# Optimization experiments

Hardware: AMD Instinct MI355X
Metric: run time of the kernel (lower is better)

Reference implementation:

```python
import jax, jax.numpy as jnp
import numpy as np

B, T, H = 64, 320, 256
D = 2 * H  # input_size; cat([cw, cell]) has dim 2*D which must equal 4*H


def setup_inputs() -> dict:
    key = jax.random.key(0)
    ks = jax.random.split(key, 10)
    sD = 1.0 / np.sqrt(D)
    sG = 1.0 / np.sqrt(2 * D)
    sH = 1.0 / np.sqrt(H)
    f32 = jnp.float32
    n = lambda k, shape, s: jax.random.normal(k, shape, dtype=f32) * s
    return {
        "v": n(ks[0], (B, T, D), 1.0),
        "W1": n(ks[1], (D, D), sD), "b1": jnp.zeros((D,), f32),
        "W2": n(ks[2], (D, D), sD), "b2": jnp.zeros((D,), f32),
        "Wg": n(ks[3], (2 * D, 2 * D), sG), "bg": jnp.zeros((2 * D,), f32),
        "Wih_f": n(ks[4], (3 * H, 2 * D), sG), "Whh_f": n(ks[5], (3 * H, H), sH),
        "bih_f": jnp.zeros((3 * H,), f32), "bhh_f": jnp.zeros((3 * H,), f32),
        "Wih_b": n(ks[6], (3 * H, 2 * D), sG), "Whh_b": n(ks[7], (3 * H, H), sH),
        "bih_b": jnp.zeros((3 * H,), f32), "bhh_b": jnp.zeros((3 * H,), f32),
    }


def _gru_cell(x, h, Wih, Whh, bih, bhh):
    # torch GRUCell math: gates ordered (r, z, n)
    gi = x @ Wih.T + bih          # (B, 3H)
    gh = h @ Whh.T + bhh          # (B, 3H)
    i_r, i_z, i_n = jnp.split(gi, 3, axis=-1)
    h_r, h_z, h_n = jnp.split(gh, 3, axis=-1)
    r = jax.nn.sigmoid(i_r + h_r)
    z = jax.nn.sigmoid(i_z + h_z)
    n = jnp.tanh(i_n + r * h_n)
    return (1.0 - z) * n + z * h


def reference(v, W1, b1, W2, b2, Wg, bg,
              Wih_f, Whh_f, bih_f, bhh_f,
              Wih_b, Whh_b, bih_b, bhh_b):
    # context_mult = linear2(v) is identical every timestep -> hoist out of loop
    cm = jnp.einsum('btd,ed->bte', v, W2) + b2          # (B, T, D)

    def step(carry, cw):
        hf, hb = carry                                   # (B, H) each
        cwm = cw @ W1.T + b1                             # (B, D)
        f = jnp.tanh(cwm[:, None, :] + cm)               # (B, T, D)
        scores = jnp.einsum('bd,btd->bt', cw, f)         # (B, T)
        attn = jax.nn.softmax(scores, axis=-1)
        cell = jnp.einsum('bt,btd->bd', attn, v)         # (B, D)
        pg = jnp.concatenate([cw, cell], axis=-1)        # (B, 2D) == (B, 4H)
        gate = jax.nn.sigmoid(pg @ Wg.T + bg)
        gi = pg * gate
        # length-1 bidirectional GRU step: each direction sees the same input
        hf2 = _gru_cell(gi, hf, Wih_f, Whh_f, bih_f, bhh_f)
        hb2 = _gru_cell(gi, hb, Wih_b, Whh_b, bih_b, bhh_b)
        return (hf2, hb2), jnp.concatenate([hf2, hb2], axis=-1)

    h0 = jnp.zeros((v.shape[0], H), v.dtype)
    _, hs = jax.lax.scan(step, (h0, h0), jnp.swapaxes(v, 0, 1))
    return hs  # (T, B, 2H)
```

## Files before the change

kernel.cpp:

```cpp
#include <hip/hip_runtime.h>

typedef unsigned short u16;
typedef __fp16 h2 __attribute__((ext_vector_type(2)));
typedef __attribute__((ext_vector_type(8))) short bf16x8;
typedef __attribute__((ext_vector_type(4))) float f32x4;

__device__ __forceinline__ float fast_exp(float x) { return __expf(x); }
__device__ __forceinline__ float fast_rcp(float x) { return __builtin_amdgcn_rcpf(x); }
__device__ __forceinline__ float fast_tanh(float x) {
  float e = fast_exp(2.0f * x);
  return 1.0f - 2.0f * fast_rcp(e + 1.0f);
}
__device__ __forceinline__ float fast_sigmoid(float x) {
  return fast_rcp(1.0f + fast_exp(-x));
}
__device__ __forceinline__ u16 f2bf(float x) {
  unsigned u = __float_as_uint(x);
  return (u16)((u + 0x7fffu + ((u >> 16) & 1u)) >> 16);
}

__global__ __launch_bounds__(256)
void k_cvt(const float* __restrict__ src, u16* __restrict__ dst, int n4)
{
  int i = blockIdx.x * 256 + threadIdx.x;
  if (i < n4) {
    float4 x = ((const float4*)src)[i];
    ushort4 o;
    o.x = f2bf(x.x); o.y = f2bf(x.y); o.z = f2bf(x.z); o.w = f2bf(x.w);
    ((ushort4*)dst)[i] = o;
  }
}

template<int EXPOUT>
__global__ __launch_bounds__(256)
void k_gemm(const float* __restrict__ A1, int K1, int map1,
            const float* __restrict__ W,
            const float* __restrict__ bias,
            float* __restrict__ C, int N, int K, int Tc, int t0)
{
  __shared__ float As[16][128];
  __shared__ float Bs[16][128];
  const int tid = threadIdx.x;
  const int m0 = blockIdx.x * 128;
  const int n0 = blockIdx.y * 128;
  const int q = tid & 3;

  const float* pA1[2];
  const float* pW[2];
#pragma unroll
  for (int r = 0; r < 2; ++r) {
    int row = m0 + r * 64 + (tid >> 2);
    int ar1 = map1 ? ((row / Tc) * 320 + t0 + row % Tc) : row;
    pA1[r] = A1 + (size_t)ar1 * K1;
    pW[r] = W + (size_t)(n0 + r * 64 + (tid >> 2)) * K;
  }

  float acc[8][8];
#pragma unroll
  for (int i = 0; i < 8; ++i)
#pragma unroll
    for (int j = 0; j < 8; ++j) acc[i][j] = 0.f;
  const int tm = (tid & 15) * 8;
  const int tn = (tid >> 4) * 8;

  for (int k0 = 0; k0 < K; k0 += 16) {
#pragma unroll
    for (int r = 0; r < 2; ++r) {
      int row = r * 64 + (tid >> 2);
      int kk = k0 + q * 4;
      float4 x = *(const float4*)(pA1[r] + kk);
      As[q * 4 + 0][row] = x.x;
      As[q * 4 + 1][row] = x.y;
      As[q * 4 + 2][row] = x.z;
      As[q * 4 + 3][row] = x.w;
      float4 y = *(const float4*)(pW[r] + kk);
      Bs[q * 4 + 0][row] = y.x;
      Bs[q * 4 + 1][row] = y.y;
      Bs[q * 4 + 2][row] = y.z;
      Bs[q * 4 + 3][row] = y.w;
    }
    __syncthreads();
#pragma unroll
    for (int k = 0; k < 16; ++k) {
      float a[8], b[8];
      *(float4*)&a[0] = *(const float4*)&As[k][tm];
      *(float4*)&a[4] = *(const float4*)&As[k][tm + 4];
      *(float4*)&b[0] = *(const float4*)&Bs[k][tn];
      *(float4*)&b[4] = *(const float4*)&Bs[k][tn + 4];
#pragma unroll
      for (int i = 0; i < 8; ++i)
#pragma unroll
        for (int j = 0; j < 8; ++j) acc[i][j] += a[i] * b[j];
    }
    __syncthreads();
  }
#pragma unroll
  for (int i = 0; i < 8; ++i) {
    int m = m0 + tm + i;
    float* Crow = C + (size_t)m * N + n0 + tn;
#pragma unroll
    for (int j = 0; j < 8; ++j) {
      float x = acc[i][j] + bias[n0 + tn + j];
      Crow[j] = EXPOUT ? fast_exp(2.0f * x) : x;
    }
  }
}

template<int MODE>
__global__ __launch_bounds__(256)
void k_mgemm(const u16* __restrict__ A1, int K1, int map1,
             const u16* __restrict__ A2,
             const u16* __restrict__ W16, const float* __restrict__ bias,
             const float* __restrict__ E1, const float* __restrict__ E2,
             void* __restrict__ Cout, int N, int K, int Tc, int t0)
{
  __shared__ alignas(16) u16 As[128][40];
  __shared__ alignas(16) u16 Bs[128][40];
  const int tid = threadIdx.x;
  const int m0 = blockIdx.x * 128;
  const int n0 = blockIdx.y * 128;
  const int wave = tid >> 6, lane = tid & 63;
  const int wm = (wave & 1) * 64, wn = (wave >> 1) * 64;
  const int K2 = K - K1;

  const u16* pA1r[2];
  const u16* pA2r[2];
  const u16* pWr[2];
#pragma unroll
  for (int r = 0; r < 2; ++r) {
    int row = r * 64 + (tid >> 2);
    int gm = m0 + row;
    int ar1 = map1 ? ((gm / Tc) * 320 + t0 + gm % Tc) : gm;
    pA1r[r] = A1 + (size_t)ar1 * K1;
    pA2r[r] = A2 ? (A2 + (size_t)gm * K2) : pA1r[r];
    pWr[r] = W16 + (size_t)(n0 + row) * K;
  }

  f32x4 acc[4][4];
#pragma unroll
  for (int a = 0; a < 4; ++a)
#pragma unroll
    for (int b = 0; b < 4; ++b) acc[a][b] = (f32x4){0.f, 0.f, 0.f, 0.f};

  const int lrow = lane & 15, lq = lane >> 4;

  for (int k0 = 0; k0 < K; k0 += 32) {
#pragma unroll
    for (int r = 0; r < 2; ++r) {
      int row = r * 64 + (tid >> 2);
      int kk = k0 + (tid & 3) * 8;
      const u16* s = (kk < K1) ? (pA1r[r] + kk) : (pA2r[r] + (kk - K1));
      *(int4*)&As[row][(tid & 3) * 8] = *(const int4*)s;
      *(int4*)&Bs[row][(tid & 3) * 8] = *(const int4*)(pWr[r] + kk);
    }
    __syncthreads();
    bf16x8 av[4], bv[4];
#pragma unroll
    for (int f = 0; f < 4; ++f) {
      av[f] = *(const bf16x8*)&As[wm + f * 16 + lrow][lq * 8];
      bv[f] = *(const bf16x8*)&Bs[wn + f * 16 + lrow][lq * 8];
    }
#pragma unroll
    for (int mf = 0; mf < 4; ++mf)
#pragma unroll
      for (int nf = 0; nf < 4; ++nf)
        acc[mf][nf] = __builtin_amdgcn_mfma_f32_16x16x32_bf16(
            av[mf], bv[nf], acc[mf][nf], 0, 0, 0);
    __syncthreads();
  }

  const int c = lane & 15, rg = lane >> 4;
#pragma unroll
  for (int mf = 0; mf < 4; ++mf) {
#pragma unroll
    for (int r = 0; r < 4; ++r) {
      int m = m0 + wm + mf * 16 + rg * 4 + r;
      int vrow = map1 ? ((m / Tc) * 320 + t0 + m % Tc) : m;
#pragma unroll
      for (int nf = 0; nf < 4; ++nf) {
        int n = n0 + wn + nf * 16 + c;
        float x = acc[mf][nf][r] + bias[n];
        if (MODE == 1) {
          float pg = (n < 512) ? E1[(size_t)vrow * 512 + n]
                               : E2[(size_t)m * 512 + (n - 512)];
          ((u16*)Cout)[(size_t)m * N + n] = f2bf(pg * fast_sigmoid(x));
        } else {
          ((float*)Cout)[(size_t)m * N + n] = x;
        }
      }
    }
  }
}

__global__ __launch_bounds__(256)
void k_scores(const float* __restrict__ v, const float* __restrict__ Ecwm,
              const float* __restrict__ Fcm, float* __restrict__ sc,
              int Tc, int t0)
{
  __shared__ float vs[32][68], fs[32][68], cs[32][68];
  const int b = blockIdx.x;
  const int tl0 = blockIdx.y * 32;
  const int s0 = blockIdx.z * 32;
  const int tid = threadIdx.x;
  const int tx = tid & 15, ty = tid >> 4;
  const float* srcV = v    + ((size_t)b * 320 + t0 + tl0) * 512;
  const float* srcF = Ecwm + ((size_t)b * Tc + tl0) * 512;
  const float* srcC = Fcm  + ((size_t)b * 320 + s0) * 512;
  float a00 = 0, a01 = 0, a10 = 0, a11 = 0;
  float vs0 = 0, vs1 = 0;
  for (int d0 = 0; d0 < 512; d0 += 64) {
#pragma unroll
    for (int r = 0; r < 2; ++r) {
      int f = r * 256 + tid;
      int row = f >> 4, qq = f & 15;
      *(float4*)&vs[row][qq * 4] = *(const float4*)(srcV + (size_t)row * 512 + d0 + qq * 4);
      *(float4*)&fs[row][qq * 4] = *(const float4*)(srcF + (size_t)row * 512 + d0 + qq * 4);
      *(float4*)&cs[row][qq * 4] = *(const float4*)(srcC + (size_t)row * 512 + d0 + qq * 4);
    }
    __syncthreads();
#pragma unroll 4
    for (int d = 0; d < 64; ++d) {
      float c0 = cs[tx][d], c1 = cs[tx + 16][d];
      float e0 = fs[ty][d], e1 = fs[ty + 16][d];
      float v0 = vs[ty][d], v1 = vs[ty + 16][d];
      vs0 += v0; vs1 += v1;
      a00 = fmaf(v0, fast_rcp(fmaf(e0, c0, 1.0f)), a00);
      a01 = fmaf(v0, fast_rcp(fmaf(e0, c1, 1.0f)), a01);
      a10 = fmaf(v1, fast_rcp(fmaf(e1, c0, 1.0f)), a10);
      a11 = fmaf(v1, fast_rcp(fmaf(e1, c1, 1.0f)), a11);
    }
    __syncthreads();
  }
  float* o = sc + (size_t)b * Tc * 320;
  o[(size_t)(tl0 + ty) * 320 + s0 + tx]           = vs0 - 2.0f * a00;
  o[(size_t)(tl0 + ty) * 320 + s0 + tx + 16]      = vs0 - 2.0f * a01;
  o[(size_t)(tl0 + ty + 16) * 320 + s0 + tx]      = vs1 - 2.0f * a10;
  o[(size_t)(tl0 + ty + 16) * 320 + s0 + tx + 16] = vs1 - 2.0f * a11;
}

__global__ __launch_bounds__(256)
void k_softmax(float* __restrict__ sc)
{
  int wave = threadIdx.x >> 6;
  int lane = threadIdx.x & 63;
  int row = blockIdx.x * 4 + wave;
  float* p = sc + (size_t)row * 320;
  float x[5];
  float mx = -1e30f;
#pragma unroll
  for (int j = 0; j < 5; ++j) { x[j] = p[lane + 64 * j]; mx = fmaxf(mx, x[j]); }
#pragma unroll
  for (int off = 32; off > 0; off >>= 1) mx = fmaxf(mx, __shfl_xor(mx, off));
  float s = 0.f;
#pragma unroll
  for (int j = 0; j < 5; ++j) { x[j] = fast_exp(x[j] - mx); s += x[j]; }
#pragma unroll
  for (int off = 32; off > 0; off >>= 1) s += __shfl_xor(s, off);
  float rinv = fast_rcp(s);
#pragma unroll
  for (int j = 0; j < 5; ++j) p[lane + 64 * j] = x[j] * rinv;
}

__global__ __launch_bounds__(256)
void k_cell(const float* __restrict__ attn, const float* __restrict__ v,
            float* __restrict__ cell, u16* __restrict__ cell16, int Tc)
{
  __shared__ float As[16][32], Bs[16][64];
  const int b = blockIdx.x;
  const int m0 = blockIdx.y * 32;
  const int n0 = blockIdx.z * 64;
  const int tid = threadIdx.x;
  const float* A = attn + (size_t)b * Tc * 320;
  const float* B = v + (size_t)b * 320 * 512;
  float acc[2][4];
#pragma unroll
  for (int i = 0; i < 2; ++i)
#pragma unroll
    for (int j = 0; j < 4; ++j) acc[i][j] = 0.f;
  const int tm = (tid & 15) * 2, tn = (tid >> 4) * 4;
  for (int k0 = 0; k0 < 320; k0 += 16) {
    if (tid < 128) {
      int row = tid >> 2, q = tid & 3;
      float4 x = *(const float4*)(A + (size_t)(m0 + row) * 320 + k0 + q * 4);
      As[q * 4 + 0][row] = x.x;
      As[q * 4 + 1][row] = x.y;
      As[q * 4 + 2][row] = x.z;
      As[q * 4 + 3][row] = x.w;
    }
    {
      int krow = tid >> 4, qq = tid & 15;
      *(float4*)&Bs[krow][qq * 4] =
          *(const float4*)(B + (size_t)(k0 + krow) * 512 + n0 + qq * 4);
    }
    __syncthreads();
#pragma unroll
    for (int k = 0; k < 16; ++k) {
      float a0 = As[k][tm], a1 = As[k][tm + 1];
      float bb[4];
      *(float4*)&bb[0] = *(const float4*)&Bs[k][tn];
#pragma unroll
      for (int j = 0; j < 4; ++j) { acc[0][j] += a0 * bb[j]; acc[1][j] += a1 * bb[j]; }
    }
    __syncthreads();
  }
#pragma unroll
  for (int i = 0; i < 2; ++i) {
    size_t off = ((size_t)b * Tc + m0 + tm + i) * 512 + n0 + tn;
    float4 o = make_float4(acc[i][0], acc[i][1], acc[i][2], acc[i][3]);
    *(float4*)(cell + off) = o;
    ushort4 o16;
    o16.x = f2bf(o.x); o16.y = f2bf(o.y); o16.z = f2bf(o.z); o16.w = f2bf(o.w);
    *(ushort4*)(cell16 + off) = o16;
  }
}

__global__ __launch_bounds__(512)
void k_recur(const float* __restrict__ GIf, const float* __restrict__ GIb,
             const float* __restrict__ Whh_f, const float* __restrict__ Whh_b,
             const float* __restrict__ bhh_f, const float* __restrict__ bhh_b,
             float* __restrict__ out, float* __restrict__ hstate,
             int Tc, int t0, int init)
{
  const int b = blockIdx.x >> 1;
  const int dir = blockIdx.x & 1;
  const int tid = threadIdx.x;
  const int i = tid & 255;
  const int half = __builtin_amdgcn_readfirstlane(tid >> 8);
  const int lane = tid & 63;

  __shared__ float part[3][256];
  __shared__ alignas(8) __fp16 hh16[256];

  const float* Wh  = dir ? Whh_b : Whh_f;
  const float* bhh = dir ? bhh_b : bhh_f;
  const float* GI  = (dir ? GIb : GIf) + (size_t)b * Tc * 768;

  h2 wr[64], wz[64], wn[64];
  {
    const float* Wr = Wh + (size_t)i * 256 + half * 128;
    const float* Wz = Wh + (size_t)(256 + i) * 256 + half * 128;
    const float* Wn = Wh + (size_t)(512 + i) * 256 + half * 128;
#pragma unroll
    for (int qd = 0; qd < 32; ++qd) {
      float4 x = *(const float4*)(Wr + 4 * qd);
      wr[2 * qd]     = __builtin_amdgcn_cvt_pkrtz(x.x, x.y);
      wr[2 * qd + 1] = __builtin_amdgcn_cvt_pkrtz(x.z, x.w);
      float4 y = *(const float4*)(Wz + 4 * qd);
      wz[2 * qd]     = __builtin_amdgcn_cvt_pkrtz(y.x, y.y);
      wz[2 * qd + 1] = __builtin_amdgcn_cvt_pkrtz(y.z, y.w);
      float4 zv = *(const float4*)(Wn + 4 * qd);
      wn[2 * qd]     = __builtin_amdgcn_cvt_pkrtz(zv.x, zv.y);
      wn[2 * qd + 1] = __builtin_amdgcn_cvt_pkrtz(zv.z, zv.w);
    }
  }

  float br = 0.f, bz = 0.f, bn = 0.f, hown = 0.f;
  if (half == 0) {
    br = bhh[i]; bz = bhh[256 + i]; bn = bhh[512 + i];
    hown = init ? 0.f : hstate[(size_t)blockIdx.x * 256 + i];
    hh16[i] = (__fp16)hown;
  }
  float* op = out + (size_t)t0 * 32768 + (size_t)b * 512 + dir * 256 + i;
  __syncthreads();

  int2 hp = *(const int2*)((const char*)hh16 + 8 * lane);

  for (int t = 0; t < Tc; ++t) {
    const float* gi = GI + (size_t)t * 768;
    float gr = 0.f, gz = 0.f, gn = 0.f;
    if (half == 0) { gr = gi[i]; gz = gi[256 + i]; gn = gi[512 + i]; }

    float ar = 0.f, az = 0.f, an = 0.f;
    const int lbase = half * 32;
#pragma unroll
    for (int p = 0; p < 64; ++p) {
      int src = (p & 1) ? hp.y : hp.x;
      h2 hh = __builtin_bit_cast(h2, __builtin_amdgcn_readlane(src, lbase + (p >> 1)));
      ar = __builtin_amdgcn_fdot2(wr[p], hh, ar, false);
      az = __builtin_amdgcn_fdot2(wz[p], hh, az, false);
      an = __builtin_amdgcn_fdot2(wn[p], hh, an, false);
    }
    if (half == 1) {
      part[0][i] = ar; part[1][i] = az; part[2][i] = an;
    }
    __syncthreads();
    if (half == 0) {
      float r  = fast_sigmoid(gr + ar + part[0][i] + br);
      float z  = fast_sigmoid(gz + az + part[1][i] + bz);
      float nn = fast_tanh(gn + r * (an + part[2][i] + bn));
      hown = (1.f - z) * nn + z * hown;
      op[(size_t)t * 32768] = hown;
      hh16[i] = (__fp16)hown;
    }
    __syncthreads();
    hp = *(const int2*)((const char*)hh16 + 8 * lane);
  }
  if (half == 0) hstate[(size_t)blockIdx.x * 256 + i] = hown;
}

extern "C" void kernel_launch(void* const* d_in, const int* in_sizes, int n_in,
                              void* d_out, int out_size, void* d_ws, size_t ws_size,
                              hipStream_t stream)
{
  const float* v     = (const float*)d_in[0];
  const float* W1    = (const float*)d_in[1];
  const float* b1    = (const float*)d_in[2];
  const float* W2    = (const float*)d_in[3];
  const float* b2    = (const float*)d_in[4];
  const float* Wg    = (const float*)d_in[5];
  const float* bg    = (const float*)d_in[6];
  const float* Wih_f = (const float*)d_in[7];
  const float* Whh_f = (const float*)d_in[8];
  const float* bih_f = (const float*)d_in[9];
  const float* bhh_f = (const float*)d_in[10];
  const float* Wih_b = (const float*)d_in[11];
  const float* Whh_b = (const float*)d_in[12];
  const float* bih_b = (const float*)d_in[13];
  const float* bhh_b = (const float*)d_in[14];
  float* out = (float*)d_out;
  float* w = (float*)d_ws;

  int Tc = 32;
  {
    const int cand[4] = {320, 160, 64, 32};
    for (int ci = 0; ci < 4; ++ci) {
      size_t need = 4ull * (17072128ull + 233472ull * (size_t)cand[ci]);
      if (need <= ws_size) { Tc = cand[ci]; break; }
    }
  }
  const int nc = 320 / Tc;

  float* cm     = w;
  float* hstate = w + 10485760;
  u16*  v16     = (u16*)(w + 10518528);
  u16*  Wg16    = (u16*)(w + 15761408);
  u16*  Wif16   = (u16*)(w + 16285696);
  u16*  Wib16   = (u16*)(w + 16678912);
  {
    size_t base = 17072128;
    float* cwm;  float* attn;  float* cell;  u16* cell16;  u16* gi16;
    cwm    = w + base;                                  base += (size_t)32768 * Tc;
    attn   = w + base;                                  base += (size_t)20480 * Tc;
    cell   = w + base;                                  base += (size_t)32768 * Tc;
    cell16 = (u16*)(w + base);                          base += (size_t)16384 * Tc;
    gi16   = (u16*)(w + base);                          base += (size_t)32768 * Tc;
    float* GIf = w + base;                              base += (size_t)49152 * Tc;
    float* GIb = w + base;

    k_cvt<<<(2621440 + 255) / 256, 256, 0, stream>>>(v, v16, 2621440);
    k_cvt<<<(262144 + 255) / 256, 256, 0, stream>>>(Wg, Wg16, 262144);
    k_cvt<<<(196608 + 255) / 256, 256, 0, stream>>>(Wih_f, Wif16, 196608);
    k_cvt<<<(196608 + 255) / 256, 256, 0, stream>>>(Wih_b, Wib16, 196608);

    k_gemm<1><<<dim3(160, 4), 256, 0, stream>>>(v, 512, 1, W2, b2, cm, 512, 512, 320, 0);

    for (int c = 0; c < nc; ++c) {
      const int t0 = c * Tc;
      const int Mc = 64 * Tc;
      k_gemm<1><<<dim3(Mc / 128, 4), 256, 0, stream>>>(v, 512, 1, W1, b1, cwm, 512, 512, Tc, t0);
      k_scores<<<dim3(64, Tc / 32, 10), 256, 0, stream>>>(v, cwm, cm, attn, Tc, t0);
      k_softmax<<<Mc / 4, 256, 0, stream>>>(attn);
      k_cell<<<dim3(64, Tc / 32, 8), 256, 0, stream>>>(attn, v, cell, cell16, Tc);
      k_mgemm<1><<<dim3(Mc / 128, 8), 256, 0, stream>>>(v16, 512, 1, cell16, Wg16, bg,
                                                        v, cell, gi16, 1024, 1024, Tc, t0);
      k_mgemm<0><<<dim3(Mc / 128, 6), 256, 0, stream>>>(gi16, 1024, 0, nullptr, Wif16, bih_f,
                                                        nullptr, nullptr, GIf, 768, 1024, Tc, t0);
      k_mgemm<0><<<dim3(Mc / 128, 6), 256, 0, stream>>>(gi16, 1024, 0, nullptr, Wib16, bih_b,
                                                        nullptr, nullptr, GIb, 768, 1024, Tc, t0);
      k_recur<<<128, 512, 0, stream>>>(GIf, GIb, Whh_f, Whh_b, bhh_f, bhh_b,
                                       out, hstate, Tc, t0, (c == 0) ? 1 : 0);
    }
  }
}
```

Baseline: 1.820 ms.

## Use split-bf16 MFMA for W1/W2 projections and dual accumulators in recurrence

Replaces the fp32 SIMT GEMM that computes the W1 and W2 projections with an MFMA kernel. It splits both operands into bf16 high and low parts and sums three products (hi*hi, hi*lo, lo*hi), keeping accuracy close to fp32 while running on the matrix cores. Extra split passes produce hi/lo copies of v, W1 and W2, which enlarges the workspace and may lower the chosen time-chunk size. The GRU recurrence inner loop also uses two independent accumulator chains per gate to shorten the fdot2 dependency chain.

```diff
diff --git a/kernel.cpp b/kernel.cpp
--- a/kernel.cpp
+++ b/kernel.cpp
@@ -17,6 +17,9 @@
 __device__ __forceinline__ u16 f2bf(float x) {
   unsigned u = __float_as_uint(x);
   return (u16)((u + 0x7fffu + ((u >> 16) & 1u)) >> 16);
+}
+__device__ __forceinline__ float bf2f(u16 u) {
+  return __uint_as_float(((unsigned)u) << 16);
 }
 
 __global__ __launch_bounds__(256)
@@ -31,77 +34,106 @@
   }
 }
 
+__global__ __launch_bounds__(256)
+void k_split(const float* __restrict__ src, u16* __restrict__ hi,
+             u16* __restrict__ lo, int n4)
+{
+  int i = blockIdx.x * 256 + threadIdx.x;
+  if (i < n4) {
+    float4 x = ((const float4*)src)[i];
+    ushort4 h, l;
+    h.x = f2bf(x.x); l.x = f2bf(x.x - bf2f(h.x));
+    h.y = f2bf(x.y); l.y = f2bf(x.y - bf2f(h.y));
+    h.z = f2bf(x.z); l.z = f2bf(x.z - bf2f(h.z));
+    h.w = f2bf(x.w); l.w = f2bf(x.w - bf2f(h.w));
+    ((ushort4*)hi)[i] = h;
+    ((ushort4*)lo)[i] = l;
+  }
+}
+
 template<int EXPOUT>
 __global__ __launch_bounds__(256)
-void k_gemm(const float* __restrict__ A1, int K1, int map1,
-            const float* __restrict__ W,
-            const float* __restrict__ bias,
-            float* __restrict__ C, int N, int K, int Tc, int t0)
-{
-  __shared__ float As[16][128];
-  __shared__ float Bs[16][128];
+void k_sgemm(const u16* __restrict__ Ahi, const u16* __restrict__ Alo,
+             const u16* __restrict__ Whi, const u16* __restrict__ Wlo,
+             const float* __restrict__ bias,
+             float* __restrict__ C, int N, int K, int Tc, int t0)
+{
+  __shared__ alignas(16) u16 Ah[128][40];
+  __shared__ alignas(16) u16 Al[128][40];
+  __shared__ alignas(16) u16 Bh[128][40];
+  __shared__ alignas(16) u16 Bl[128][40];
   const int tid = threadIdx.x;
   const int m0 = blockIdx.x * 128;
   const int n0 = blockIdx.y * 128;
-  const int q = tid & 3;
-
-  const float* pA1[2];
-  const float* pW[2];
+  const int wave = tid >> 6, lane = tid & 63;
+  const int wm = (wave & 1) * 64, wn = (wave >> 1) * 64;
+
+  const u16 *pAh[2], *pAl[2], *pBh[2], *pBl[2];
 #pragma unroll
   for (int r = 0; r < 2; ++r) {
-    int row = m0 + r * 64 + (tid >> 2);
-    int ar1 = map1 ? ((row / Tc) * 320 + t0 + row % Tc) : row;
-    pA1[r] = A1 + (size_t)ar1 * K1;
-    pW[r] = W + (size_t)(n0 + r * 64 + (tid >> 2)) * K;
-  }
-
-  float acc[8][8];
-#pragma unroll
-  for (int i = 0; i < 8; ++i)
-#pragma unroll
-    for (int j = 0; j < 8; ++j) acc[i][j] = 0.f;
-  const int tm = (tid & 15) * 8;
-  const int tn = (tid >> 4) * 8;
-
-  for (int k0 = 0; k0 < K; k0 += 16) {
+    int row = r * 64 + (tid >> 2);
+    int gm = m0 + row;
+    int ar = (gm / Tc) * 320 + t0 + gm % Tc;
+    pAh[r] = Ahi + (size_t)ar * K;
+    pAl[r] = Alo + (size_t)ar * K;
+    int gn = n0 + row;
+    pBh[r] = Whi + (size_t)gn * K;
+    pBl[r] = Wlo + (size_t)gn * K;
+  }
+
+  f32x4 acc[4][4];
+#pragma unroll
+  for (int a = 0; a < 4; ++a)
+#pragma unroll
+    for (int b = 0; b < 4; ++b) acc[a][b] = (f32x4){0.f, 0.f, 0.f, 0.f};
+
+  const int lrow = lane & 15, lq = lane >> 4;
+
+  for (int k0 = 0; k0 < K; k0 += 32) {
 #pragma unroll
     for (int r = 0; r < 2; ++r) {
       int row = r * 64 + (tid >> 2);
-      int kk = k0 + q * 4;
-      float4 x = *(const float4*)(pA1[r] + kk);
-      As[q * 4 + 0][row] = x.x;
-      As[q * 4 + 1][row] = x.y;
-      As[q * 4 + 2][row] = x.z;
-      As[q * 4 + 3][row] = x.w;
-      float4 y = *(const float4*)(pW[r] + kk);
-      Bs[q * 4 + 0][row] = y.x;
-      Bs[q * 4 + 1][row] = y.y;
-      Bs[q * 4 + 2][row] = y.z;
-      Bs[q * 4 + 3][row] = y.w;
-    }
-    __syncthreads();
-#pragma unroll
-    for (int k = 0; k < 16; ++k) {
-      float a[8], b[8];
-      *(float4*)&a[0] = *(const float4*)&As[k][tm];
-      *(float4*)&a[4] = *(const float4*)&As[k][tm + 4];
-      *(float4*)&b[0] = *(const float4*)&Bs[k][tn];
-      *(float4*)&b[4] = *(const float4*)&Bs[k][tn + 4];
-#pragma unroll
-      for (int i = 0; i < 8; ++i)
-#pragma unroll
-        for (int j = 0; j < 8; ++j) acc[i][j] += a[i] * b[j];
-    }
-    __syncthreads();
-  }
-#pragma unroll
-  for (int i = 0; i < 8; ++i) {
-    int m = m0 + tm + i;
-    float* Crow = C + (size_t)m * N + n0 + tn;
-#pragma unroll
-    for (int j = 0; j < 8; ++j) {
-      float x = acc[i][j] + bias[n0 + tn + j];
-      Crow[j] = EXPOUT ? fast_exp(2.0f * x) : x;
+      int kk = k0 + (tid & 3) * 8;
+      *(int4*)&Ah[row][(tid & 3) * 8] = *(const int4*)(pAh[r] + kk);
+      *(int4*)&Al[row][(tid & 3) * 8] = *(const int4*)(pAl[r] + kk);
+      *(int4*)&Bh[row][(tid & 3) * 8] = *(const int4*)(pBh[r] + kk);
+      *(int4*)&Bl[row][(tid & 3) * 8] = *(const int4*)(pBl[r] + kk);
+    }
+    __syncthreads();
+    bf16x8 avh[4], avl[4], bvh[4], bvl[4];
+#pragma unroll
+    for (int f = 0; f < 4; ++f) {
+      avh[f] = *(const bf16x8*)&Ah[wm + f * 16 + lrow][lq * 8];
+      avl[f] = *(const bf16x8*)&Al[wm + f * 16 + lrow][lq * 8];
+      bvh[f] = *(const bf16x8*)&Bh[wn + f * 16 + lrow][lq * 8];
+      bvl[f] = *(const bf16x8*)&Bl[wn + f * 16 + lrow][lq * 8];
+    }
+#pragma unroll
+    for (int mf = 0; mf < 4; ++mf)
+#pragma unroll
+      for (int nf = 0; nf < 4; ++nf) {
+        acc[mf][nf] = __builtin_amdgcn_mfma_f32_16x16x32_bf16(
+            avh[mf], bvh[nf], acc[mf][nf], 0, 0, 0);
+        acc[mf][nf] = __builtin_amdgcn_mfma_f32_16x16x32_bf16(
+            avh[mf], bvl[nf], acc[mf][nf], 0, 0, 0);
+        acc[mf][nf] = __builtin_amdgcn_mfma_f32_16x16x32_bf16(
+            avl[mf], bvh[nf], acc[mf][nf], 0, 0, 0);
+      }
+    __syncthreads();
+  }
+
+  const int c = lane & 15, rg = lane >> 4;
+#pragma unroll
+  for (int mf = 0; mf < 4; ++mf) {
+#pragma unroll
+    for (int r = 0; r < 4; ++r) {
+      int m = m0 + wm + mf * 16 + rg * 4 + r;
+#pragma unroll
+      for (int nf = 0; nf < 4; ++nf) {
+        int n = n0 + wn + nf * 16 + c;
+        float x = acc[mf][nf][r] + bias[n];
+        C[(size_t)m * N + n] = EXPOUT ? fast_exp(2.0f * x) : x;
+      }
     }
   }
 }
@@ -370,16 +402,21 @@
     float gr = 0.f, gz = 0.f, gn = 0.f;
     if (half == 0) { gr = gi[i]; gz = gi[256 + i]; gn = gi[512 + i]; }
 
-    float ar = 0.f, az = 0.f, an = 0.f;
+    float ar0 = 0.f, az0 = 0.f, an0 = 0.f;
+    float ar1 = 0.f, az1 = 0.f, an1 = 0.f;
     const int lbase = half * 32;
 #pragma unroll
-    for (int p = 0; p < 64; ++p) {
-      int src = (p & 1) ? hp.y : hp.x;
-      h2 hh = __builtin_bit_cast(h2, __builtin_amdgcn_readlane(src, lbase + (p >> 1)));
-      ar = __builtin_amdgcn_fdot2(wr[p], hh, ar, false);
-      az = __builtin_amdgcn_fdot2(wz[p], hh, az, false);
-      an = __builtin_amdgcn_fdot2(wn[p], hh, an, false);
-    }
+    for (int p = 0; p < 64; p += 2) {
+      h2 h0 = __builtin_bit_cast(h2, __builtin_amdgcn_readlane(hp.x, lbase + (p >> 1)));
+      h2 h1 = __builtin_bit_cast(h2, __builtin_amdgcn_readlane(hp.y, lbase + (p >> 1)));
+      ar0 = __builtin_amdgcn_fdot2(wr[p], h0, ar0, false);
+      az0 = __builtin_amdgcn_fdot2(wz[p], h0, az0, false);
+      an0 = __builtin_amdgcn_fdot2(wn[p], h0, an0, false);
+      ar1 = __builtin_amdgcn_fdot2(wr[p + 1], h1, ar1, false);
+      az1 = __builtin_amdgcn_fdot2(wz[p + 1], h1, az1, false);
+      an1 = __builtin_amdgcn_fdot2(wn[p + 1], h1, an1, false);
+    }
+    float ar = ar0 + ar1, az = az0 + az1, an = an0 + an1;
     if (half == 1) {
       part[0][i] = ar; part[1][i] = az; part[2][i] = an;
     }
@@ -424,7 +461,7 @@
   {
     const int cand[4] = {320, 160, 64, 32};
     for (int ci = 0; ci < 4; ++ci) {
-      size_t need = 4ull * (17072128ull + 233472ull * (size_t)cand[ci]);
+      size_t need = 4ull * (22839296ull + 233472ull * (size_t)cand[ci]);
       if (need <= ws_size) { Tc = cand[ci]; break; }
     }
   }
@@ -432,12 +469,17 @@
 
   float* cm     = w;
   float* hstate = w + 10485760;
-  u16*  v16     = (u16*)(w + 10518528);
-  u16*  Wg16    = (u16*)(w + 15761408);
-  u16*  Wif16   = (u16*)(w + 16285696);
-  u16*  Wib16   = (u16*)(w + 16678912);
+  u16*  vhi     = (u16*)(w + 10518528);
+  u16*  vlo     = (u16*)(w + 15761408);
+  u16*  Wg16    = (u16*)(w + 21004288);
+  u16*  Wif16   = (u16*)(w + 21528576);
+  u16*  Wib16   = (u16*)(w + 21921792);
+  u16*  W1hi    = (u16*)(w + 22315008);
+  u16*  W1lo    = (u16*)(w + 22446080);
+  u16*  W2hi    = (u16*)(w + 22577152);
+  u16*  W2lo    = (u16*)(w + 22708224);
   {
-    size_t base = 17072128;
+    size_t base = 22839296;
     float* cwm;  float* attn;  float* cell;  u16* cell16;  u16* gi16;
     cwm    = w + base;                                  base += (size_t)32768 * Tc;
     attn   = w + base;                                  base += (size_t)20480 * Tc;
@@ -447,21 +489,25 @@
     float* GIf = w + base;                              base += (size_t)49152 * Tc;
     float* GIb = w + base;
 
-    k_cvt<<<(2621440 + 255) / 256, 256, 0, stream>>>(v, v16, 2621440);
+    k_split<<<(2621440 + 255) / 256, 256, 0, stream>>>(v, vhi, vlo, 2621440);
+    k_split<<<(65536 + 255) / 256, 256, 0, stream>>>(W1, W1hi, W1lo, 65536);
+    k_split<<<(65536 + 255) / 256, 256, 0, stream>>>(W2, W2hi, W2lo, 65536);
     k_cvt<<<(262144 + 255) / 256, 256, 0, stream>>>(Wg, Wg16, 262144);
     k_cvt<<<(196608 + 255) / 256, 256, 0, stream>>>(Wih_f, Wif16, 196608);
     k_cvt<<<(196608 + 255) / 256, 256, 0, stream>>>(Wih_b, Wib16, 196608);
 
-    k_gemm<1><<<dim3(160, 4), 256, 0, stream>>>(v, 512, 1, W2, b2, cm, 512, 512, 320, 0);
+    k_sgemm<1><<<dim3(160, 4), 256, 0, stream>>>(vhi, vlo, W2hi, W2lo, b2,
+                                                 cm, 512, 512, 320, 0);
 
     for (int c = 0; c < nc; ++c) {
       const int t0 = c * Tc;
       const int Mc = 64 * Tc;
-      k_gemm<1><<<dim3(Mc / 128, 4), 256, 0, stream>>>(v, 512, 1, W1, b1, cwm, 512, 512, Tc, t0);
+      k_sgemm<1><<<dim3(Mc / 128, 4), 256, 0, stream>>>(vhi, vlo, W1hi, W1lo, b1,
+                                                        cwm, 512, 512, Tc, t0);
       k_scores<<<dim3(64, Tc / 32, 10), 256, 0, stream>>>(v, cwm, cm, attn, Tc, t0);
       k_softmax<<<Mc / 4, 256, 0, stream>>>(attn);
       k_cell<<<dim3(64, Tc / 32, 8), 256, 0, stream>>>(attn, v, cell, cell16, Tc);
-      k_mgemm<1><<<dim3(Mc / 128, 8), 256, 0, stream>>>(v16, 512, 1, cell16, Wg16, bg,
+      k_mgemm<1><<<dim3(Mc / 128, 8), 256, 0, stream>>>(vhi, 512, 1, cell16, Wg16, bg,
                                                         v, cell, gi16, 1024, 1024, Tc, t0);
       k_mgemm<0><<<dim3(Mc / 128, 6), 256, 0, stream>>>(gi16, 1024, 0, nullptr, Wif16, bih_f,
                                                         nullptr, nullptr, GIf, 768, 1024, Tc, t0);
```

Result: faster. 1.564 ms (-14.1%).
